# Kernel optimization log

Hardware: AMD Instinct MI355X
Metric: run time of the kernel (lower is better)

## Reference

```python
import jax, jax.numpy as jnp
import numpy as np

MASK_VALUE = -1e10  # matches module's -10000000000.0


def setup_inputs() -> dict:
    key = jax.random.key(0)
    k1, k2, k3, k4, k5 = jax.random.split(key, 5)
    B, NQ, NKV, D = 32, 32, 8, 128
    NUM_PAGES, TPP, PAGES_PER_SLOT = 4096, 16, 128
    query = jax.random.normal(k1, (B, 1, NQ, D), dtype=jnp.float32)
    key_pages = jax.random.normal(k2, (NKV, NUM_PAGES, TPP, D), dtype=jnp.float32)
    value_pages = jax.random.normal(k3, (NKV, NUM_PAGES, TPP, D), dtype=jnp.float32)
    page_map = jax.random.randint(k4, (B, PAGES_PER_SLOT), 0, NUM_PAGES, dtype=jnp.int32)
    seq_lengths = jax.random.randint(k5, (B,), 1, PAGES_PER_SLOT * TPP + 1, dtype=jnp.int32)
    return {
        "query": query,
        "key_pages": key_pages,
        "value_pages": value_pages,
        "page_map": page_map,
        "seq_lengths": seq_lengths,
    }


def reference(query, key_pages, value_pages, page_map, seq_lengths):
    """Paged attention, decode mode (single query token per sequence, GQA).

    query:       [B, 1, NQ, D]
    key_pages:   [NKV, NUM_PAGES, TPP, D]
    value_pages: [NKV, NUM_PAGES, TPP, D]
    page_map:    [B, P] page indices per sequence
    seq_lengths: [B] valid kv tokens per sequence
    """
    B, _, NQ, D = query.shape
    NKV, _, TPP, _ = key_pages.shape
    G = NQ // NKV  # GQA group size
    # take last query position -> [B, NKV, G, D]
    q = query[:, -1].reshape(B, NKV, G, D)
    # gather pages per sequence: [NKV, B, P, TPP, D] -> [B, NKV, S, D]
    k = jnp.moveaxis(key_pages[:, page_map], 0, 1).reshape(B, NKV, -1, D)
    v = jnp.moveaxis(value_pages[:, page_map], 0, 1).reshape(B, NKV, -1, D)
    S = k.shape[2]
    scores = jnp.einsum("bkgd,bksd->bkgs", q, k)  # [B, NKV, G, S]
    valid = jnp.arange(S)[None, :] < seq_lengths[:, None]  # [B, S]
    scores = jnp.where(valid[:, None, None, :], scores, MASK_VALUE)
    weights = jax.nn.softmax(scores, axis=-1)
    out = jnp.einsum("bkgs,bksd->bkgd", weights, v)  # [B, NKV, G, D]
    return out.reshape(B, 1, NQ, D)
```

## Files before the change

### kernel.cpp

```cpp
#include <hip/hip_runtime.h>
#include <math.h>

#define NB      32
#define NKV     8
#define NQ      32
#define GQ      4
#define DH      128
#define TPP     16
#define PPS     128
#define NPAGES  4096
#define NSPLIT  16
#define NBK     (NB*NKV)
#define PAGE_F  (TPP*DH)
#define PART_F  (GQ*DH + 2*GQ)

__global__ __launch_bounds__(256) void pa_partial(
    const float* __restrict__ query,
    const float* __restrict__ key_pages,
    const float* __restrict__ value_pages,
    const int*   __restrict__ page_map,
    const int*   __restrict__ seq_lengths,
    float*       __restrict__ ws)
{
    const int blk = blockIdx.x;
    const int sp  = blk & (NSPLIT - 1);
    const int bk  = blk >> 4;
    const int kv  = bk & (NKV - 1);
    const int b   = bk >> 3;
    const int tid = threadIdx.x;

    const int seq     = seq_lengths[b];
    const int n_pages = (seq + TPP - 1) / TPP;
    if (sp >= n_pages) return;

    const int grp = tid >> 4;
    const int l16 = tid & 15;
    const int c0  = l16 * 4;
    const int c1  = 64 + l16 * 4;

    float qreg[GQ][8];
    #pragma unroll
    for (int g = 0; g < GQ; ++g) {
        const float* qb = query + (size_t)((b * NQ + kv * GQ + g) * DH);
        const float4 a = *(const float4*)(qb + c0);
        const float4 c = *(const float4*)(qb + c1);
        qreg[g][0] = a.x; qreg[g][1] = a.y; qreg[g][2] = a.z; qreg[g][3] = a.w;
        qreg[g][4] = c.x; qreg[g][5] = c.y; qreg[g][6] = c.z; qreg[g][7] = c.w;
    }

    const float* kbase = key_pages   + (size_t)kv * NPAGES * PAGE_F;
    const float* vbase = value_pages + (size_t)kv * NPAGES * PAGE_F;
    const int*   pmap  = page_map + b * PPS;

    float m[GQ] = {-1e30f, -1e30f, -1e30f, -1e30f};
    float l[GQ] = {0.f, 0.f, 0.f, 0.f};
    float acc[GQ][8] = {};

    float4 ck0, ck1, cv0, cv1;
    {
        const size_t ro = (size_t)pmap[sp] * PAGE_F + grp * DH;
        ck0 = *(const float4*)(kbase + ro + c0);
        ck1 = *(const float4*)(kbase + ro + c1);
        cv0 = *(const float4*)(vbase + ro + c0);
        cv1 = *(const float4*)(vbase + ro + c1);
    }

    for (int p = sp; p < n_pages; p += NSPLIT) {
        float4 nk0, nk1, nv0, nv1;
        const int pn = p + NSPLIT;
        if (pn < n_pages) {
            const size_t ro = (size_t)pmap[pn] * PAGE_F + grp * DH;
            nk0 = *(const float4*)(kbase + ro + c0);
            nk1 = *(const float4*)(kbase + ro + c1);
            nv0 = *(const float4*)(vbase + ro + c0);
            nv1 = *(const float4*)(vbase + ro + c1);
        }

        const float kx[8] = {ck0.x, ck0.y, ck0.z, ck0.w, ck1.x, ck1.y, ck1.z, ck1.w};
        float s[GQ];
        #pragma unroll
        for (int g = 0; g < GQ; ++g) {
            float t = qreg[g][0]*kx[0] + qreg[g][1]*kx[1] + qreg[g][2]*kx[2] + qreg[g][3]*kx[3]
                    + qreg[g][4]*kx[4] + qreg[g][5]*kx[5] + qreg[g][6]*kx[6] + qreg[g][7]*kx[7];
            #pragma unroll
            for (int off = 8; off >= 1; off >>= 1) t += __shfl_xor(t, off);
            s[g] = t;
        }

        const bool valid = (p * TPP + grp) < seq;
        const float vx[8] = {cv0.x, cv0.y, cv0.z, cv0.w, cv1.x, cv1.y, cv1.z, cv1.w};

        #pragma unroll
        for (int g = 0; g < GQ; ++g) {
            const float mn = fmaxf(m[g], s[g]);
            float pc = __expf(s[g] - mn);
            pc = valid ? pc : 0.f;
            const float sc = __expf(m[g] - mn);
            m[g] = mn;
            l[g] = l[g] * sc + pc;
            #pragma unroll
            for (int j = 0; j < 8; ++j)
                acc[g][j] = acc[g][j] * sc + pc * vx[j];
        }

        ck0 = nk0; ck1 = nk1; cv0 = nv0; cv1 = nv1;
    }

    __shared__ float s_acc[16][GQ][DH];
    __shared__ float s_m[16][GQ];
    __shared__ float s_l[16][GQ];

    #pragma unroll
    for (int g = 0; g < GQ; ++g) {
        *(float4*)&s_acc[grp][g][c0] = make_float4(acc[g][0], acc[g][1], acc[g][2], acc[g][3]);
        *(float4*)&s_acc[grp][g][c1] = make_float4(acc[g][4], acc[g][5], acc[g][6], acc[g][7]);
    }
    if (l16 == 0) {
        #pragma unroll
        for (int g = 0; g < GQ; ++g) { s_m[grp][g] = m[g]; s_l[grp][g] = l[g]; }
    }
    __syncthreads();

    const int d  = tid & 127;
    const int gA = tid >> 7;
    const int gB = gA + 2;

    float MA = -1e30f, MB = -1e30f;
    #pragma unroll
    for (int i = 0; i < 16; ++i) {
        MA = fmaxf(MA, s_m[i][gA]);
        MB = fmaxf(MB, s_m[i][gB]);
    }
    float LA = 0.f, LB = 0.f, oA = 0.f, oB = 0.f;
    #pragma unroll
    for (int i = 0; i < 16; ++i) {
        const float eA = __expf(s_m[i][gA] - MA);
        const float eB = __expf(s_m[i][gB] - MB);
        LA += s_l[i][gA] * eA;
        LB += s_l[i][gB] * eB;
        oA += s_acc[i][gA][d] * eA;
        oB += s_acc[i][gB][d] * eB;
    }

    float* base = ws + (size_t)(bk * NSPLIT + sp) * PART_F;
    base[gA * DH + d] = oA;
    base[gB * DH + d] = oB;
    if (d == 0) {
        base[GQ * DH + gA]      = MA;
        base[GQ * DH + GQ + gA] = LA;
        base[GQ * DH + gB]      = MB;
        base[GQ * DH + GQ + gB] = LB;
    }
}

__global__ __launch_bounds__(256) void pa_combine(
    const float* __restrict__ ws,
    const int*   __restrict__ seq_lengths,
    float*       __restrict__ out)
{
    const int blk = blockIdx.x;
    const int b   = blk >> 3;
    const int kv  = blk & 7;
    const int tid = threadIdx.x;
    const int d   = tid & 127;
    const int gA  = tid >> 7;
    const int gB  = gA + 2;

    const int seq     = seq_lengths[b];
    const int n_pages = (seq + TPP - 1) / TPP;
    const int ns      = (n_pages < NSPLIT) ? n_pages : NSPLIT;

    const float* base0 = ws + (size_t)blk * NSPLIT * PART_F;

    float MA = -1e30f, MB = -1e30f;
    for (int si = 0; si < ns; ++si) {
        const float* p = base0 + si * PART_F;
        MA = fmaxf(MA, p[GQ * DH + gA]);
        MB = fmaxf(MB, p[GQ * DH + gB]);
    }

    float LA = 0.f, LB = 0.f, oA = 0.f, oB = 0.f;
    for (int si = 0; si < ns; ++si) {
        const float* p = base0 + si * PART_F;
        const float eA = __expf(p[GQ * DH + gA] - MA);
        const float eB = __expf(p[GQ * DH + gB] - MB);
        LA += p[GQ * DH + GQ + gA] * eA;
        LB += p[GQ * DH + GQ + gB] * eB;
        oA += p[gA * DH + d] * eA;
        oB += p[gB * DH + d] * eB;
    }

    float* ob = out + (size_t)(b * NQ + kv * GQ) * DH;
    ob[gA * DH + d] = oA / LA;
    ob[gB * DH + d] = oB / LB;
}

extern "C" void kernel_launch(void* const* d_in, const int* in_sizes, int n_in,
                              void* d_out, int out_size, void* d_ws, size_t ws_size,
                              hipStream_t stream)
{
    const float* query       = (const float*)d_in[0];
    const float* key_pages   = (const float*)d_in[1];
    const float* value_pages = (const float*)d_in[2];
    const int*   page_map    = (const int*)d_in[3];
    const int*   seq_lengths = (const int*)d_in[4];
    float*       out         = (float*)d_out;
    float*       ws          = (float*)d_ws;

    pa_partial<<<NBK * NSPLIT, 256, 0, stream>>>(
        query, key_pages, value_pages, page_map, seq_lengths, ws);
    pa_combine<<<NBK, 256, 0, stream>>>(ws, seq_lengths, out);
}
```

Before: 59.53 us.

## Use exp2 softmax with deferred rescaling, DPP reductions, and prefetched page indices

Folds log2(e) into the query so every exponent becomes a native exp2, and swaps the shuffle-based 16-lane reduction for DPP row operations. The online-softmax rescale of m, l and acc now runs only when some lane's score exceeds the running max by a threshold, so most iterations skip it. The next page index is loaded one iteration early to take the page_map load off the dependent address chain. The deferred rescale lets exp values grow up to 2^8 before renormalising, which is meant to stay within float range, and the wave-wide vote adds a branch.

```diff
diff --git a/kernel.cpp b/kernel.cpp
--- a/kernel.cpp
+++ b/kernel.cpp
@@ -13,6 +13,27 @@
 #define NBK     (NB*NKV)
 #define PAGE_F  (TPP*DH)
 #define PART_F  (GQ*DH + 2*GQ)
+#define LOG2E   1.44269504088896340736f
+#define DEFER_THR 8.0f
+
+#if __has_builtin(__builtin_amdgcn_exp2f)
+#define EXP2(x) __builtin_amdgcn_exp2f(x)
+#else
+#define EXP2(x) exp2f(x)
+#endif
+
+template<int CTRL>
+__device__ __forceinline__ float dpp_addf(float x) {
+    int y = __builtin_amdgcn_update_dpp(0, __float_as_int(x), CTRL, 0xF, 0xF, true);
+    return x + __int_as_float(y);
+}
+__device__ __forceinline__ float sum16(float x) {
+    x = dpp_addf<0xB1>(x);
+    x = dpp_addf<0x4E>(x);
+    x = dpp_addf<0x141>(x);
+    x = dpp_addf<0x140>(x);
+    return x;
+}
 
 __global__ __launch_bounds__(256) void pa_partial(
     const float* __restrict__ query,
@@ -44,8 +65,10 @@
         const float* qb = query + (size_t)((b * NQ + kv * GQ + g) * DH);
         const float4 a = *(const float4*)(qb + c0);
         const float4 c = *(const float4*)(qb + c1);
-        qreg[g][0] = a.x; qreg[g][1] = a.y; qreg[g][2] = a.z; qreg[g][3] = a.w;
-        qreg[g][4] = c.x; qreg[g][5] = c.y; qreg[g][6] = c.z; qreg[g][7] = c.w;
+        qreg[g][0] = a.x * LOG2E; qreg[g][1] = a.y * LOG2E;
+        qreg[g][2] = a.z * LOG2E; qreg[g][3] = a.w * LOG2E;
+        qreg[g][4] = c.x * LOG2E; qreg[g][5] = c.y * LOG2E;
+        qreg[g][6] = c.z * LOG2E; qreg[g][7] = c.w * LOG2E;
     }
 
     const float* kbase = key_pages   + (size_t)kv * NPAGES * PAGE_F;
@@ -56,6 +79,7 @@
     float l[GQ] = {0.f, 0.f, 0.f, 0.f};
     float acc[GQ][8] = {};
 
+    int pg_nxt = (sp + NSPLIT < n_pages) ? pmap[sp + NSPLIT] : 0;
     float4 ck0, ck1, cv0, cv1;
     {
         const size_t ro = (size_t)pmap[sp] * PAGE_F + grp * DH;
@@ -69,38 +93,38 @@
         float4 nk0, nk1, nv0, nv1;
         const int pn = p + NSPLIT;
         if (pn < n_pages) {
-            const size_t ro = (size_t)pmap[pn] * PAGE_F + grp * DH;
+            const size_t ro = (size_t)pg_nxt * PAGE_F + grp * DH;
             nk0 = *(const float4*)(kbase + ro + c0);
             nk1 = *(const float4*)(kbase + ro + c1);
             nv0 = *(const float4*)(vbase + ro + c0);
             nv1 = *(const float4*)(vbase + ro + c1);
+            pg_nxt = (pn + NSPLIT < n_pages) ? pmap[pn + NSPLIT] : 0;
         }
 
+        const bool valid = (p * TPP + grp) < seq;
         const float kx[8] = {ck0.x, ck0.y, ck0.z, ck0.w, ck1.x, ck1.y, ck1.z, ck1.w};
-        float s[GQ];
+        const float vx[8] = {cv0.x, cv0.y, cv0.z, cv0.w, cv1.x, cv1.y, cv1.z, cv1.w};
+
         #pragma unroll
         for (int g = 0; g < GQ; ++g) {
             float t = qreg[g][0]*kx[0] + qreg[g][1]*kx[1] + qreg[g][2]*kx[2] + qreg[g][3]*kx[3]
                     + qreg[g][4]*kx[4] + qreg[g][5]*kx[5] + qreg[g][6]*kx[6] + qreg[g][7]*kx[7];
+            float s2 = sum16(t);
+            s2 = valid ? s2 : -INFINITY;
+
+            const bool need = s2 > m[g] + DEFER_THR;
+            if (__any(need)) {
+                const float mn = need ? s2 : m[g];
+                const float sc = EXP2(m[g] - mn);
+                m[g] = mn;
+                l[g] *= sc;
+                #pragma unroll
+                for (int j = 0; j < 8; ++j) acc[g][j] *= sc;
+            }
+            const float pc = EXP2(s2 - m[g]);
+            l[g] += pc;
             #pragma unroll
-            for (int off = 8; off >= 1; off >>= 1) t += __shfl_xor(t, off);
-            s[g] = t;
-        }
-
-        const bool valid = (p * TPP + grp) < seq;
-        const float vx[8] = {cv0.x, cv0.y, cv0.z, cv0.w, cv1.x, cv1.y, cv1.z, cv1.w};
-
-        #pragma unroll
-        for (int g = 0; g < GQ; ++g) {
-            const float mn = fmaxf(m[g], s[g]);
-            float pc = __expf(s[g] - mn);
-            pc = valid ? pc : 0.f;
-            const float sc = __expf(m[g] - mn);
-            m[g] = mn;
-            l[g] = l[g] * sc + pc;
-            #pragma unroll
-            for (int j = 0; j < 8; ++j)
-                acc[g][j] = acc[g][j] * sc + pc * vx[j];
+            for (int j = 0; j < 8; ++j) acc[g][j] += pc * vx[j];
         }
 
         ck0 = nk0; ck1 = nk1; cv0 = nv0; cv1 = nv1;
@@ -134,8 +158,8 @@
     float LA = 0.f, LB = 0.f, oA = 0.f, oB = 0.f;
     #pragma unroll
     for (int i = 0; i < 16; ++i) {
-        const float eA = __expf(s_m[i][gA] - MA);
-        const float eB = __expf(s_m[i][gB] - MB);
+        const float eA = EXP2(s_m[i][gA] - MA);
+        const float eB = EXP2(s_m[i][gB] - MB);
         LA += s_l[i][gA] * eA;
         LB += s_l[i][gB] * eB;
         oA += s_acc[i][gA][d] * eA;
@@ -182,8 +206,8 @@
     float LA = 0.f, LB = 0.f, oA = 0.f, oB = 0.f;
     for (int si = 0; si < ns; ++si) {
         const float* p = base0 + si * PART_F;
-        const float eA = __expf(p[GQ * DH + gA] - MA);
-        const float eB = __expf(p[GQ * DH + gB] - MB);
+        const float eA = EXP2(p[GQ * DH + gA] - MA);
+        const float eB = EXP2(p[GQ * DH + gB] - MB);
         LA += p[GQ * DH + GQ + gA] * eA;
         LB += p[GQ * DH + GQ + gB] * eB;
         oA += p[gA * DH + d] * eA;
```

Result: faster. 56.13 us (-5.7%).
